# Kernel optimization log

Measured on AMD Instinct MI355X. Metric: run time of the kernel, lower is better.

## Reference

```python
import jax, jax.numpy as jnp
import numpy as np
from jax import lax

WL = 140      # window_length
OFC = 118     # ofc_channel = window_length - 21 - 1
TDN = 21      # TimeDelayNum (sliding time-delay count)
D_CM = 16     # cm_attn embed dim
N_BR = 4      # conv_eeg_audio_number
C_OUT = 10    # conv_output_channel
KS = 9        # conv kernel size

def _init(key, shape, fan_in):
    return jax.random.uniform(key, shape, jnp.float32, -1.0, 1.0) / np.sqrt(fan_in)

def setup_inputs():
    key = jax.random.key(0)
    ks = jax.random.split(key, 12)
    return {
        "x": jax.random.normal(ks[0], (1, 1, 18, WL), dtype=jnp.float32),
        "tdA_in_w": _init(ks[1], (3 * OFC, OFC), OFC),
        "tdA_in_b": jnp.zeros((3 * OFC,), jnp.float32),
        "tdA_out_w": _init(ks[2], (OFC, OFC), OFC),
        "tdA_out_b": jnp.zeros((OFC,), jnp.float32),
        "tdB_in_w": _init(ks[3], (3 * OFC, OFC), OFC),
        "tdB_in_b": jnp.zeros((3 * OFC,), jnp.float32),
        "tdB_out_w": _init(ks[4], (OFC, OFC), OFC),
        "tdB_out_b": jnp.zeros((OFC,), jnp.float32),
        "cm_in_w": _init(ks[5], (N_BR, 3 * D_CM, D_CM), D_CM),
        "cm_in_b": jnp.zeros((N_BR, 3 * D_CM), jnp.float32),
        "cm_out_w": _init(ks[6], (N_BR, D_CM, D_CM), D_CM),
        "cm_out_b": jnp.zeros((N_BR, D_CM), jnp.float32),
        "projA_w": _init(ks[7], (16, 1), 1),
        "projB_w": _init(ks[8], (16, 1), 1),
        "conv_w": _init(ks[9], (N_BR, C_OUT, 16, KS), 16 * KS),
        "conv_b": jnp.zeros((N_BR, C_OUT), jnp.float32),
        "fc1_w": _init(ks[10], (40, 40), 40),
        "fc1_b": jnp.zeros((40,), jnp.float32),
        "fc2_w": _init(ks[11], (2, 40), 40),
        "fc2_b": jnp.zeros((2,), jnp.float32),
    }

def _mha(q, k, v, in_w, in_b, out_w, out_b):
    # single-head attention; q: (Lq, d), k/v: (Lk, d) -> (Lq, d)
    d = q.shape[-1]
    wq, wk, wv = jnp.split(in_w, 3, axis=0)
    bq, bk, bv = jnp.split(in_b, 3)
    qp = (q @ wq.T + bq) * (1.0 / np.sqrt(d))
    kp = k @ wk.T + bk
    vp = v @ wv.T + bv
    attn = jax.nn.softmax(qp @ kp.T, axis=-1)
    return (attn @ vp) @ out_w.T + out_b

def _forward(x, tdA_in_w, tdA_in_b, tdA_out_w, tdA_out_b,
             tdB_in_w, tdB_in_b, tdB_out_w, tdB_out_b,
             cm_in_w, cm_in_b, cm_out_w, cm_out_b,
             projA_w, projB_w, conv_w, conv_b,
             fc1_w, fc1_b, fc2_w, fc2_b):
    sig = x[0, 0]                               # (18, 140)
    wavA_raw, eeg_raw, wavB_raw = sig[0], sig[1:17], sig[17]
    # ChannelWav: sliding time-delay unfold -> (TDN, OFC)
    idx = jnp.arange(TDN)[:, None] + jnp.arange(OFC)[None, :]
    kA = wavA_raw[idx]                          # (21, 118)
    kB = wavB_raw[idx]
    eeg = eeg_raw[:, WL - OFC:]                 # (16, 118)
    # time-delay attention (embed_dim = 118, seq = 16 eeg channels / 21 delays)
    attA = _mha(eeg, kA, kA, tdA_in_w, tdA_in_b, tdA_out_w, tdA_out_b)  # (16, 118)
    attB = _mha(eeg, kB, kB, tdB_in_w, tdB_in_b, tdB_out_w, tdB_out_b)
    # select_max: pick attention row with largest total correlation to eeg
    iA = jnp.argmax(jnp.sum(eeg @ attA.T, axis=1))
    iB = jnp.argmax(jnp.sum(eeg @ attB.T, axis=1))
    wA = projA_w @ attA[iA][None, :]            # 1x1 conv == outer product, (16, 118)
    wB = projB_w @ attB[iB][None, :]
    data = [wA, eeg, eeg, wB]
    kv = [eeg, wA, wB, eeg]
    feats = []
    for i in range(N_BR):                       # 4 structurally distinct branches
        o = _mha(data[i].T, kv[i].T, kv[i].T,
                 cm_in_w[i], cm_in_b[i], cm_out_w[i], cm_out_b[i])      # (118, 16)
        y = lax.conv_general_dilated(o.T[None], conv_w[i], (1,), 'VALID')  # (1, 10, 110)
        y = jax.nn.relu(y[0] + conv_b[i][:, None])
        feats.append(jnp.max(y, axis=-1))       # AdaptiveMaxPool1d(1) -> (10,)
    flat = jnp.concatenate(feats)               # (40,)
    h = jax.nn.sigmoid(flat @ fc1_w.T + fc1_b)
    out = jax.nn.sigmoid(h @ fc2_w.T + fc2_b)
    return out[None, :]                         # (1, 2)

def reference(x, tdA_in_w, tdA_in_b, tdA_out_w, tdA_out_b,
              tdB_in_w, tdB_in_b, tdB_out_w, tdB_out_b,
              cm_in_w, cm_in_b, cm_out_w, cm_out_b,
              projA_w, projB_w, conv_w, conv_b,
              fc1_w, fc1_b, fc2_w, fc2_b):
    return _forward(x, tdA_in_w, tdA_in_b, tdA_out_w, tdA_out_b,
                    tdB_in_w, tdB_in_b, tdB_out_w, tdB_out_b,
                    cm_in_w, cm_in_b, cm_out_w, cm_out_b,
                    projA_w, projB_w, conv_w, conv_b,
                    fc1_w, fc1_b, fc2_w, fc2_b)
```

## Files before the change

kernel.cpp:

```cpp
#include <hip/hip_runtime.h>
#include <math.h>

#define WL   140
#define OFC  118
#define TDN  21
#define COUT 10
#define KS   9
#define IW_SZ (OFC * OFC)

#define PROJ_STRIDE 6848
#define KP_OFF      1888
#define VP_OFF      4368
#define WS_ATT_A    13696
#define WS_ATT_B    13824
#define WS_FEATS    13952
#define WS_FLAGS    14080

#define MAGIC 0x1F2E3D4C
#define NSLOTS 18

struct Params {
    const float *x;
    const float *tdA_in_w, *tdA_in_b, *tdA_out_w, *tdA_out_b;
    const float *tdB_in_w, *tdB_in_b, *tdB_out_w, *tdB_out_b;
    const float *cm_in_w, *cm_in_b, *cm_out_w, *cm_out_b;
    const float *projA_w, *projB_w, *conv_w, *conv_b;
    const float *fc1_w, *fc1_b, *fc2_w, *fc2_b;
    float *ws, *out;
};

struct TdSm {
    float wpad[59][122];
    float inp[21][120];
    float owpad[OFC][122];
    float qpp[16][122];
    float kpp[TDN][122];
    float vpp[TDN][122];
    float attn[16][22];
    float acs[22];
    float avcs[120];
    float colsum[120];
    float Ssum[16];
    float avsel[120];
    int   sel;
};

struct BrSm {
    float arow[120];
    float pv[16];
    float eeg_s[16][OFC];
    float w_inT[16][48];
    float b_in[48];
    float tv[3][16];
    float w_out[16][16];
    float b_out[16];
    float cw[COUT * 16 * KS];
    float cb[COUT];
    float kpS[OFC][17];
    float vpS[OFC][17];
    float u[120], v2[120];
    float part_m[4][128];
    float part_l[4][128];
    float part_acc[4][OFC][17];
    float o2[OFC][17];
    float qpS[OFC][17];
    float a_[120], dvec[120];
    float Avec[16], Bvec[16];
    float Gc[COUT][KS], cb2[COUT];
    float y[COUT][22];
};

struct HdSm { float f[64]; float h[64]; };

union alignas(16) Sm { TdSm t; BrSm b; HdSm h; };

__device__ inline float wred(float v) {
    #pragma unroll
    for (int off = 32; off; off >>= 1) v += __shfl_xor(v, off);
    return v;
}

__device__ inline void postM(int* f, int tid) {
    __syncthreads();
    if (tid == 0)
        __hip_atomic_store(f, MAGIC, __ATOMIC_RELEASE, __HIP_MEMORY_SCOPE_AGENT);
}

__device__ inline void waitM(int* base, int first, int n, int tid) {
    if (tid == 0) {
        for (int i = 0; i < n; ++i) {
            int* f = base + (first + i) * 16;
            while (__hip_atomic_load(f, __ATOMIC_RELAXED, __HIP_MEMORY_SCOPE_AGENT) != MAGIC)
                __builtin_amdgcn_s_sleep(1);
        }
        __builtin_amdgcn_fence(__ATOMIC_ACQUIRE, "agent");
    }
    __syncthreads();
}

__device__ void td_proj(int blk, int tid, const Params& p, TdSm& s)
{
    const int b    = blk / 6;
    const int rem  = blk % 6;
    const int sec  = rem >> 1;
    const int half = rem & 1;
    const float* in_w = (b ? p.tdB_in_w : p.tdA_in_w) + sec * IW_SZ + half * 59 * OFC;
    const float* in_b = (b ? p.tdB_in_b : p.tdA_in_b) + sec * OFC + half * 59;
    const float* wav  = p.x + (b ? 17 * WL : 0);

    for (int e = tid; e < 59 * 59; e += 512) {
        int o = e / 59, j = e - o * 59;
        ((float2*)&s.wpad[o][0])[j] = ((const float2*)(in_w + o * OFC))[j];
    }
    if (sec == 0) {
        for (int e = tid; e < 16 * OFC; e += 512) {
            int r = e / OFC, c = e - (e / OFC) * OFC;
            s.inp[r][c] = p.x[(1 + r) * WL + (WL - OFC) + c];
        }
    } else {
        for (int e = tid; e < TDN * 120; e += 512) {
            int t = e / 120, j = e - (e / 120) * 120;
            s.inp[t][j] = wav[t + j];
        }
    }
    __syncthreads();

    const int   R     = (sec == 0) ? 16 : TDN;
    const float scale = (sec == 0) ? (1.0f / sqrtf(118.0f)) : 1.0f;
    float* dst = p.ws + b * PROJ_STRIDE
               + (sec == 0 ? 0 : (sec == 1 ? KP_OFF : VP_OFF));

    for (int e = tid; e < R * 59; e += 512) {
        int r = e / 59, o = e - r * 59;
        const float2* a  = (const float2*)&s.inp[r][0];
        const float2* w2 = (const float2*)&s.wpad[o][0];
        float s0 = 0.f;
        #pragma unroll 4
        for (int j = 0; j < 59; ++j) {
            float2 u = a[j], w = w2[j];
            s0 += u.x * w.x + u.y * w.y;
        }
        dst[r * OFC + half * 59 + o] = (s0 + in_b[o]) * scale;
    }
}

__device__ void td_phase2(int b, int tid, const Params& p, TdSm& s)
{
    const float* base  = p.ws + b * PROJ_STRIDE;
    const float* out_b = b ? p.tdB_out_b : p.tdA_out_b;
    const int wid = tid >> 6, lane = tid & 63;

    for (int e = tid; e < 16 * 59; e += 512) {
        int r = e / 59, j = e - r * 59;
        ((float2*)&s.qpp[r][0])[j] = ((const float2*)(base + r * OFC))[j];
    }
    for (int e = tid; e < TDN * 59; e += 512) {
        int t = e / 59, j = e - t * 59;
        ((float2*)&s.kpp[t][0])[j] = ((const float2*)(base + KP_OFF + t * OFC))[j];
        ((float2*)&s.vpp[t][0])[j] = ((const float2*)(base + VP_OFF + t * OFC))[j];
    }
    __syncthreads();

    if (tid < 16 * TDN) {
        int i = tid / TDN, t = tid - (tid / TDN) * TDN;
        const float2* q = (const float2*)&s.qpp[i][0];
        const float2* k = (const float2*)&s.kpp[t][0];
        float sc = 0.f;
        #pragma unroll 4
        for (int j = 0; j < 59; ++j) {
            float2 u = q[j], v = k[j];
            sc += u.x * v.x + u.y * v.y;
        }
        s.attn[i][t] = sc;
    }
    __syncthreads();

    if (tid < 16) {
        float m = s.attn[tid][0];
        for (int t = 1; t < TDN; ++t) m = fmaxf(m, s.attn[tid][t]);
        float l = 0.f;
        for (int t = 0; t < TDN; ++t) {
            float pp = __expf(s.attn[tid][t] - m);
            s.attn[tid][t] = pp;
            l += pp;
        }
        float inv = 1.f / l;
        for (int t = 0; t < TDN; ++t) s.attn[tid][t] *= inv;
    }
    __syncthreads();

    if (tid < TDN) {
        float a = 0.f;
        for (int i = 0; i < 16; ++i) a += s.attn[i][tid];
        s.acs[tid] = a;
    }
    __syncthreads();

    if (tid < OFC) {
        float a = 0.f;
        for (int t = 0; t < TDN; ++t) a += s.acs[t] * s.vpp[t][tid];
        s.avcs[tid] = a;
    }
    __syncthreads();

    if (tid < OFC) {
        const float2* a  = (const float2*)&s.avcs[0];
        const float2* w2 = (const float2*)&s.owpad[tid][0];
        float a0 = 0.f;
        #pragma unroll 4
        for (int j = 0; j < 59; ++j) {
            float2 u = a[j], v = w2[j];
            a0 += u.x * v.x + u.y * v.y;
        }
        s.colsum[tid] = a0 + 16.f * out_b[tid];
    }
    __syncthreads();

    for (int d = wid; d < 16; d += 8) {
        const float* er = p.x + (1 + d) * WL + (WL - OFC);
        int j0 = lane * 2;
        float sc = 0.f;
        if (j0 < OFC) {
            float2 ev = *(const float2*)(er + j0);
            float2 cv = *(const float2*)(&s.colsum[j0]);
            sc = ev.x * cv.x + ev.y * cv.y;
        }
        sc = wred(sc);
        if (lane == 0) s.Ssum[d] = sc;
    }
    __syncthreads();

    if (tid == 0) {
        int best = 0; float bv = s.Ssum[0];
        for (int i = 1; i < 16; ++i)
            if (s.Ssum[i] > bv) { bv = s.Ssum[i]; best = i; }
        s.sel = best;
    }
    __syncthreads();

    if (tid < OFC) {
        float a = 0.f;
        for (int t = 0; t < TDN; ++t) a += s.attn[s.sel][t] * s.vpp[t][tid];
        s.avsel[tid] = a;
    }
    __syncthreads();

    if (tid < OFC) {
        const float2* a  = (const float2*)&s.avsel[0];
        const float2* w2 = (const float2*)&s.owpad[tid][0];
        float a0 = 0.f;
        #pragma unroll 4
        for (int j = 0; j < 59; ++j) {
            float2 u = a[j], v = w2[j];
            a0 += u.x * v.x + u.y * v.y;
        }
        p.ws[(b ? WS_ATT_B : WS_ATT_A) + tid] = a0 + out_b[tid];
    }
}

__device__ void br_pre(int br, int tid, const Params& p, BrSm& s)
{
    const bool d_r1 = (br == 0 || br == 3);

    for (int e = tid; e < 16 * OFC; e += 512) {
        int r = e / OFC, c = e - (e / OFC) * OFC;
        s.eeg_s[r][c] = p.x[(1 + r) * WL + (WL - OFC) + c];
    }
    for (int e = tid; e < 768; e += 512) {
        int q = e / 16, r = e % 16;
        s.w_inT[r][q] = p.cm_in_w[br * 768 + e];
    }
    if (tid < 48) s.b_in[tid] = p.cm_in_b[br * 48 + tid];
    if (tid >= 64 && tid < 320) {
        int e = tid - 64;
        s.w_out[e >> 4][e & 15] = p.cm_out_w[br * 256 + e];
    }
    if (tid >= 384 && tid < 400) s.b_out[tid - 384] = p.cm_out_b[br * 16 + (tid - 384)];
    for (int e = tid; e < COUT * 16 * KS; e += 512) s.cw[e] = p.conv_w[br * 1440 + e];
    if (tid >= 400 && tid < 410) s.cb[tid - 400] = p.conv_b[br * COUT + (tid - 400)];
    {
        const float* pvg = (br < 2) ? p.projA_w : p.projB_w;
        if (tid >= 416 && tid < 432) s.pv[tid - 416] = pvg[tid - 416];
    }
    __syncthreads();

    if (tid < 48) {
        float a = 0.f;
        #pragma unroll
        for (int r = 0; r < 16; ++r) a += s.pv[r] * s.w_inT[r][tid];
        s.tv[tid / 16][tid % 16] = a;
    }
    __syncthreads();

    if (d_r1) {
        for (int e = tid; e < 2 * OFC * 16; e += 512) {
            int sec01 = e / (OFC * 16);
            int rem = e - sec01 * OFC * 16;
            int j = rem >> 4, o = rem & 15;
            float a = 0.f;
            #pragma unroll
            for (int r = 0; r < 16; ++r) a += s.eeg_s[r][j] * s.w_inT[r][(1 + sec01) * 16 + o];
            a += s.b_in[(1 + sec01) * 16 + o];
            (sec01 ? &s.vpS[0][0] : &s.kpS[0][0])[j * 17 + o] = a;
        }
        __syncthreads();
        if (tid < OFC) {
            float uu = 0.f, vv = 0.f;
            #pragma unroll
            for (int o = 0; o < 16; ++o) {
                float kv = s.kpS[tid][o];
                uu += s.tv[0][o] * kv;
                vv += s.b_in[o] * kv;
            }
            s.u[tid] = uu; s.v2[tid] = vv;
        }
    } else {
        for (int e = tid; e < OFC * 16; e += 512) {
            int j = e >> 4, o = e & 15;
            float a = 0.f;
            #pragma unroll
            for (int r = 0; r < 16; ++r) a += s.eeg_s[r][j] * s.w_inT[r][o];
            s.qpS[j][o] = (a + s.b_in[o]) * 0.25f;
        }
        __syncthreads();
        if (tid < OFC) {
            float a = 0.f;
            #pragma unroll
            for (int o = 0; o < 16; ++o) a += s.qpS[tid][o] * s.tv[1][o];
            s.a_[tid] = a;
        }
        if (tid >= 128 && tid < 144) {
            int c = tid - 128;
            float A = 0.f, B = 0.f;
            #pragma unroll
            for (int o = 0; o < 16; ++o) {
                A += s.tv[2][o] * s.w_out[c][o];
                B += s.b_in[32 + o] * s.w_out[c][o];
            }
            s.Avec[c] = A;
            s.Bvec[c] = B + s.b_out[c];
        }
        __syncthreads();
        if (tid < COUT * KS) {
            int c = tid / KS, k = tid - (tid / KS) * KS;
            float g = 0.f;
            #pragma unroll
            for (int m = 0; m < 16; ++m) g += s.Avec[m] * s.cw[(c * 16 + m) * KS + k];
            s.Gc[c][k] = g;
        }
        if (tid >= 128 && tid < 128 + COUT) {
            int c = tid - 128;
            float cc = s.cb[c];
            #pragma unroll
            for (int m = 0; m < 16; ++m) {
                float bsum = 0.f;
                #pragma unroll
                for (int k = 0; k < KS; ++k) bsum += s.cw[(c * 16 + m) * KS + k];
                cc += s.Bvec[m] * bsum;
            }
            s.cb2[c] = cc;
        }
    }
}

__device__ void br_main(int br, int tid, const Params& p, BrSm& s)
{
    const bool d_r1 = (br == 0 || br == 3);
    const float* ar = p.ws + ((br < 2) ? WS_ATT_A : WS_ATT_B);
    if (tid < OFC) s.arow[tid] = ar[tid];
    __syncthreads();

    if (d_r1) {
        const int g = tid >> 7, j = tid & 127;
        float acc[16];
        float m = -INFINITY, l = 0.f;
        #pragma unroll
        for (int r = 0; r < 16; ++r) acc[r] = 0.f;

        if (j < OFC) {
            const float aj = s.arow[j];
            const int t0 = (g * OFC) >> 2, t1 = ((g + 1) * OFC) >> 2;
            for (int t = t0; t < t1; ++t) {
                float sc = 0.25f * fmaf(aj, s.u[t], s.v2[t]);
                float mn = fmaxf(m, sc);
                float c  = __expf(m - mn);
                float pp = __expf(sc - mn);
                l = l * c + pp;
                const float* vr = &s.vpS[t][0];
                #pragma unroll
                for (int r = 0; r < 16; ++r) acc[r] = acc[r] * c + pp * vr[r];
                m = mn;
            }
            s.part_m[g][j] = m;
            s.part_l[g][j] = l;
            #pragma unroll
            for (int r = 0; r < 16; ++r) s.part_acc[g][j][r] = acc[r];
        }
        __syncthreads();

        if (tid < OFC) {
            float m0 = s.part_m[0][tid], m1 = s.part_m[1][tid];
            float m2 = s.part_m[2][tid], m3 = s.part_m[3][tid];
            float mm = fmaxf(fmaxf(m0, m1), fmaxf(m2, m3));
            float c0 = __expf(m0 - mm), c1 = __expf(m1 - mm);
            float c2 = __expf(m2 - mm), c3 = __expf(m3 - mm);
            float ll = c0 * s.part_l[0][tid] + c1 * s.part_l[1][tid]
                     + c2 * s.part_l[2][tid] + c3 * s.part_l[3][tid];
            float inv = 1.f / ll;
            float orow[16];
            #pragma unroll
            for (int r = 0; r < 16; ++r)
                orow[r] = (c0 * s.part_acc[0][tid][r] + c1 * s.part_acc[1][tid][r]
                         + c2 * s.part_acc[2][tid][r] + c3 * s.part_acc[3][tid][r]) * inv;
            for (int c = 0; c < 16; ++c) {
                float a = s.b_out[c];
                #pragma unroll
                for (int d = 0; d < 16; ++d) a += orow[d] * s.w_out[c][d];
                s.o2[tid][c] = a;
            }
        }
        __syncthreads();

        if (tid < COUT * 22) {
            int c = tid / 22, grp = tid - (tid / 22) * 22;
            int pbase = grp * 5;
            float acc5[5];
            #pragma unroll
            for (int i = 0; i < 5; ++i) acc5[i] = s.cb[c];
            for (int mI = 0; mI < 16; ++mI) {
                float win[13];
                #pragma unroll
                for (int t = 0; t < 13; ++t) win[t] = s.o2[pbase + t][mI];
                #pragma unroll
                for (int k = 0; k < KS; ++k) {
                    float wv = s.cw[(c * 16 + mI) * KS + k];
                    #pragma unroll
                    for (int i = 0; i < 5; ++i) acc5[i] += win[i + k] * wv;
                }
            }
            float mx = fmaxf(fmaxf(fmaxf(acc5[0], acc5[1]), fmaxf(acc5[2], acc5[3])), acc5[4]);
            s.y[c][grp] = fmaxf(mx, 0.f);
        }
        __syncthreads();
    } else {
        if (tid < OFC) {
            const float aj = s.a_[tid];
            float m = -INFINITY;
            for (int t = 0; t < OFC; ++t) m = fmaxf(m, aj * s.arow[t]);
            float l = 0.f, d = 0.f;
            for (int t = 0; t < OFC; ++t) {
                float e = __expf(aj * s.arow[t] - m);
                l += e;
                d += e * s.arow[t];
            }
            s.dvec[tid] = d / l;
        }
        __syncthreads();

        if (tid < COUT * 22) {
            int c = tid / 22, grp = tid - (tid / 22) * 22;
            int pbase = grp * 5;
            float win[13];
            #pragma unroll
            for (int t = 0; t < 13; ++t) win[t] = s.dvec[pbase + t];
            float acc5[5];
            #pragma unroll
            for (int i = 0; i < 5; ++i) acc5[i] = s.cb2[c];
            #pragma unroll
            for (int k = 0; k < KS; ++k) {
                float wv = s.Gc[c][k];
                #pragma unroll
                for (int i = 0; i < 5; ++i) acc5[i] += win[i + k] * wv;
            }
            float mx = fmaxf(fmaxf(fmaxf(acc5[0], acc5[1]), fmaxf(acc5[2], acc5[3])), acc5[4]);
            s.y[c][grp] = fmaxf(mx, 0.f);
        }
        __syncthreads();
    }

    if (tid < COUT) {
        float mx = s.y[tid][0];
        for (int g2 = 1; g2 < 22; ++g2) mx = fmaxf(mx, s.y[tid][g2]);
        p.ws[WS_FEATS + br * COUT + tid] = mx;
    }
}

__global__ __launch_bounds__(512) void fused_net(Params p)
{
    __shared__ Sm sm;
    const int blk = blockIdx.x;
    const int tid = threadIdx.x;
    int* flags = (int*)(p.ws + WS_FLAGS);

    if (blk < 12) {
        td_proj(blk, tid, p, sm.t);
        postM(&flags[blk * 16], tid);

        if (blk < 2) {
            const float* ow = blk ? p.tdB_out_w : p.tdA_out_w;
            for (int e = tid; e < OFC * 59; e += 512) {
                int o = e / 59, j = e - o * 59;
                ((float2*)&sm.t.owpad[o][0])[j] = ((const float2*)(ow + o * OFC))[j];
            }
            waitM(flags, blk * 6, 6, tid);
            td_phase2(blk, tid, p, sm.t);
            postM(&flags[(12 + blk) * 16], tid);

            if (blk == 0) {
                waitM(flags, 14, 4, tid);
                if (tid < NSLOTS)
                    __hip_atomic_store(&flags[tid * 16], 0,
                                       __ATOMIC_RELAXED, __HIP_MEMORY_SCOPE_AGENT);
                __syncthreads();
                if (tid < 40) sm.h.f[tid] = p.ws[WS_FEATS + tid];
                __syncthreads();
                if (tid < 40) {
                    float a = p.fc1_b[tid];
                    for (int k = 0; k < 40; ++k) a += sm.h.f[k] * p.fc1_w[tid * 40 + k];
                    sm.h.h[tid] = 1.f / (1.f + __expf(-a));
                }
                __syncthreads();
                if (tid < 2) {
                    float a = p.fc2_b[tid];
                    for (int k = 0; k < 40; ++k) a += sm.h.h[k] * p.fc2_w[tid * 40 + k];
                    p.out[tid] = 1.f / (1.f + __expf(-a));
                }
            }
        }
    } else {
        const int br = blk - 12;
        br_pre(br, tid, p, sm.b);
        waitM(flags, (br < 2) ? 12 : 13, 1, tid);
        br_main(br, tid, p, sm.b);
        postM(&flags[(14 + br) * 16], tid);
    }
}

extern "C" void kernel_launch(void* const* d_in, const int* in_sizes, int n_in,
                              void* d_out, int out_size, void* d_ws, size_t ws_size,
                              hipStream_t stream) {
    Params prm;
    prm.x         = (const float*)d_in[0];
    prm.tdA_in_w  = (const float*)d_in[1];
    prm.tdA_in_b  = (const float*)d_in[2];
    prm.tdA_out_w = (const float*)d_in[3];
    prm.tdA_out_b = (const float*)d_in[4];
    prm.tdB_in_w  = (const float*)d_in[5];
    prm.tdB_in_b  = (const float*)d_in[6];
    prm.tdB_out_w = (const float*)d_in[7];
    prm.tdB_out_b = (const float*)d_in[8];
    prm.cm_in_w   = (const float*)d_in[9];
    prm.cm_in_b   = (const float*)d_in[10];
    prm.cm_out_w  = (const float*)d_in[11];
    prm.cm_out_b  = (const float*)d_in[12];
    prm.projA_w   = (const float*)d_in[13];
    prm.projB_w   = (const float*)d_in[14];
    prm.conv_w    = (const float*)d_in[15];
    prm.conv_b    = (const float*)d_in[16];
    prm.fc1_w     = (const float*)d_in[17];
    prm.fc1_b     = (const float*)d_in[18];
    prm.fc2_w     = (const float*)d_in[19];
    prm.fc2_b     = (const float*)d_in[20];
    prm.ws        = (float*)d_ws;
    prm.out       = (float*)d_out;

    fused_net<<<dim3(16), dim3(512), 0, stream>>>(prm);
}
```

Measured before the change: 38.68 us.

## Spread time-delay projections over 28 blocks with direct global-memory dot products

```diff
diff --git a/kernel.cpp b/kernel.cpp
--- a/kernel.cpp
+++ b/kernel.cpp
@@ -17,7 +17,7 @@
 #define WS_FLAGS    14080
 
 #define MAGIC 0x1F2E3D4C
-#define NSLOTS 18
+#define NSLOTS 34
 
 struct Params {
     const float *x;
@@ -26,12 +26,11 @@
     const float *cm_in_w, *cm_in_b, *cm_out_w, *cm_out_b;
     const float *projA_w, *projB_w, *conv_w, *conv_b;
     const float *fc1_w, *fc1_b, *fc2_w, *fc2_b;
+    float *fc_unused;
     float *ws, *out;
 };
 
 struct TdSm {
-    float wpad[59][122];
-    float inp[21][120];
     float owpad[OFC][122];
     float qpp[16][122];
     float kpp[TDN][122];
@@ -98,50 +97,43 @@
     __syncthreads();
 }
 
-__device__ void td_proj(int blk, int tid, const Params& p, TdSm& s)
+__device__ void td_proj_direct(int side, int lw, int lane, const Params& p)
 {
-    const int b    = blk / 6;
-    const int rem  = blk % 6;
-    const int sec  = rem >> 1;
-    const int half = rem & 1;
-    const float* in_w = (b ? p.tdB_in_w : p.tdA_in_w) + sec * IW_SZ + half * 59 * OFC;
-    const float* in_b = (b ? p.tdB_in_b : p.tdA_in_b) + sec * OFC + half * 59;
-    const float* wav  = p.x + (b ? 17 * WL : 0);
-
-    for (int e = tid; e < 59 * 59; e += 512) {
-        int o = e / 59, j = e - o * 59;
-        ((float2*)&s.wpad[o][0])[j] = ((const float2*)(in_w + o * OFC))[j];
-    }
+    int sec, o, r, R;
+    if (lw < 30) {
+        sec = 0; o = lw * 4 + (lane & 3); r = lane >> 2; R = 16;
+    } else {
+        sec = (lw < 70) ? 1 : 2;
+        int base = (lw - (sec == 1 ? 30 : 70)) * 3;
+        o = base + lane % 3; r = lane / 3; R = TDN;
+    }
+    if (o >= OFC || r >= R) return;
+
+    const float* in_w = (side ? p.tdB_in_w : p.tdA_in_w) + sec * IW_SZ + o * OFC;
+    const float  bias = (side ? p.tdB_in_b : p.tdA_in_b)[sec * OFC + o];
+    const float2* w2  = (const float2*)in_w;
+    float s0 = 0.f;
+
     if (sec == 0) {
-        for (int e = tid; e < 16 * OFC; e += 512) {
-            int r = e / OFC, c = e - (e / OFC) * OFC;
-            s.inp[r][c] = p.x[(1 + r) * WL + (WL - OFC) + c];
-        }
-    } else {
-        for (int e = tid; e < TDN * 120; e += 512) {
-            int t = e / 120, j = e - (e / 120) * 120;
-            s.inp[t][j] = wav[t + j];
-        }
-    }
-    __syncthreads();
-
-    const int   R     = (sec == 0) ? 16 : TDN;
-    const float scale = (sec == 0) ? (1.0f / sqrtf(118.0f)) : 1.0f;
-    float* dst = p.ws + b * PROJ_STRIDE
-               + (sec == 0 ? 0 : (sec == 1 ? KP_OFF : VP_OFF));
-
-    for (int e = tid; e < R * 59; e += 512) {
-        int r = e / 59, o = e - r * 59;
-        const float2* a  = (const float2*)&s.inp[r][0];
-        const float2* w2 = (const float2*)&s.wpad[o][0];
-        float s0 = 0.f;
+        const float2* a = (const float2*)(p.x + (1 + r) * WL + (WL - OFC));
         #pragma unroll 4
         for (int j = 0; j < 59; ++j) {
             float2 u = a[j], w = w2[j];
             s0 += u.x * w.x + u.y * w.y;
         }
-        dst[r * OFC + half * 59 + o] = (s0 + in_b[o]) * scale;
-    }
+        s0 = (s0 + bias) * (1.0f / sqrtf(118.0f));
+    } else {
+        const float* wr = p.x + (side ? 17 * WL : 0) + r;
+        #pragma unroll 4
+        for (int j = 0; j < 59; ++j) {
+            float2 w = w2[j];
+            s0 += wr[2 * j] * w.x + wr[2 * j + 1] * w.y;
+        }
+        s0 += bias;
+    }
+    p.ws[side * PROJ_STRIDE
+         + (sec == 0 ? 0 : (sec == 1 ? KP_OFF : VP_OFF))
+         + r * OFC + o] = s0;
 }
 
 __device__ void td_phase2(int b, int tid, const Params& p, TdSm& s)
@@ -492,48 +484,52 @@
     const int tid = threadIdx.x;
     int* flags = (int*)(p.ws + WS_FLAGS);
 
-    if (blk < 12) {
-        td_proj(blk, tid, p, sm.t);
-        postM(&flags[blk * 16], tid);
-
-        if (blk < 2) {
-            const float* ow = blk ? p.tdB_out_w : p.tdA_out_w;
-            for (int e = tid; e < OFC * 59; e += 512) {
-                int o = e / 59, j = e - o * 59;
-                ((float2*)&sm.t.owpad[o][0])[j] = ((const float2*)(ow + o * OFC))[j];
-            }
-            waitM(flags, blk * 6, 6, tid);
-            td_phase2(blk, tid, p, sm.t);
-            postM(&flags[(12 + blk) * 16], tid);
-
-            if (blk == 0) {
-                waitM(flags, 14, 4, tid);
-                if (tid < NSLOTS)
-                    __hip_atomic_store(&flags[tid * 16], 0,
-                                       __ATOMIC_RELAXED, __HIP_MEMORY_SCOPE_AGENT);
-                __syncthreads();
-                if (tid < 40) sm.h.f[tid] = p.ws[WS_FEATS + tid];
-                __syncthreads();
-                if (tid < 40) {
-                    float a = p.fc1_b[tid];
-                    for (int k = 0; k < 40; ++k) a += sm.h.f[k] * p.fc1_w[tid * 40 + k];
-                    sm.h.h[tid] = 1.f / (1.f + __expf(-a));
-                }
-                __syncthreads();
-                if (tid < 2) {
-                    float a = p.fc2_b[tid];
-                    for (int k = 0; k < 40; ++k) a += sm.h.h[k] * p.fc2_w[tid * 40 + k];
-                    p.out[tid] = 1.f / (1.f + __expf(-a));
-                }
-            }
-        }
-    } else {
-        const int br = blk - 12;
-        br_pre(br, tid, p, sm.b);
-        waitM(flags, (br < 2) ? 12 : 13, 1, tid);
-        br_main(br, tid, p, sm.b);
-        postM(&flags[(14 + br) * 16], tid);
-    }
+    if (blk >= 2 && blk < 30) {
+        const int side = (blk < 16) ? 0 : 1;
+        const int gw   = (blk - (side ? 16 : 2)) * 8 + (tid >> 6);
+        if (gw < 110) td_proj_direct(side, gw, tid & 63, p);
+        postM(&flags[(blk - 2) * 16], tid);
+        return;
+    }
+
+    if (blk < 2) {
+        const float* ow = blk ? p.tdB_out_w : p.tdA_out_w;
+        for (int e = tid; e < OFC * 59; e += 512) {
+            int o = e / 59, j = e - o * 59;
+            ((float2*)&sm.t.owpad[o][0])[j] = ((const float2*)(ow + o * OFC))[j];
+        }
+        waitM(flags, blk ? 14 : 0, 14, tid);
+        td_phase2(blk, tid, p, sm.t);
+        postM(&flags[(28 + blk) * 16], tid);
+
+        if (blk == 0) {
+            waitM(flags, 30, 4, tid);
+            if (tid < NSLOTS)
+                __hip_atomic_store(&flags[tid * 16], 0,
+                                   __ATOMIC_RELAXED, __HIP_MEMORY_SCOPE_AGENT);
+            __syncthreads();
+            if (tid < 40) sm.h.f[tid] = p.ws[WS_FEATS + tid];
+            __syncthreads();
+            if (tid < 40) {
+                float a = p.fc1_b[tid];
+                for (int k = 0; k < 40; ++k) a += sm.h.f[k] * p.fc1_w[tid * 40 + k];
+                sm.h.h[tid] = 1.f / (1.f + __expf(-a));
+            }
+            __syncthreads();
+            if (tid < 2) {
+                float a = p.fc2_b[tid];
+                for (int k = 0; k < 40; ++k) a += sm.h.h[k] * p.fc2_w[tid * 40 + k];
+                p.out[tid] = 1.f / (1.f + __expf(-a));
+            }
+        }
+        return;
+    }
+
+    const int br = blk - 30;
+    br_pre(br, tid, p, sm.b);
+    waitM(flags, (br < 2) ? 28 : 29, 1, tid);
+    br_main(br, tid, p, sm.b);
+    postM(&flags[(30 + br) * 16], tid);
 }
 
 extern "C" void kernel_launch(void* const* d_in, const int* in_sizes, int n_in,
@@ -561,8 +557,9 @@
     prm.fc1_b     = (const float*)d_in[18];
     prm.fc2_w     = (const float*)d_in[19];
     prm.fc2_b     = (const float*)d_in[20];
+    prm.fc_unused = nullptr;
     prm.ws        = (float*)d_ws;
     prm.out       = (float*)d_out;
 
-    fused_net<<<dim3(16), dim3(512), 0, stream>>>(prm);
-}
+    fused_net<<<dim3(34), dim3(512), 0, stream>>>(prm);
+}
```

Result: slower. 39.75 us (median of 2 runs) (+2.8%).
